# Kernel optimization log

Hardware: AMD Instinct MI355X
Metric: run time of the kernel (lower is better)

Reference implementation:

```python
import jax, jax.numpy as jnp
import numpy as np

DIM = 64
SQRT_DIM = np.sqrt(DIM).astype(np.float32)
NEG_INF = -1e9


def setup_inputs() -> dict:
    key = jax.random.key(0)
    kq, kk, kv, km = jax.random.split(key, 4)
    B, Q, K, D = 32, 1024, 1024, DIM
    query = jax.random.normal(kq, (B, Q, D), dtype=jnp.float32)
    k = jax.random.normal(kk, (B, K, D), dtype=jnp.float32)
    value = jax.random.normal(kv, (B, K, D), dtype=jnp.float32)
    mask = jax.random.randint(km, (B, Q, K), 0, 2).astype(jnp.bool_)
    return {"query": query, "key": k, "value": value, "mask": mask}


def reference(query, key, value, mask):
    # score: [B, Q, K]
    score = jnp.einsum('bqd,bkd->bqk', query, key) / SQRT_DIM
    score = jnp.where(mask, NEG_INF, score)
    attn = jax.nn.softmax(score, axis=-1)
    context = jnp.einsum('bqk,bkd->bqd', attn, value)
    return (context, attn)
```

## Files before the change

kernel.cpp:

```cpp
#include <hip/hip_runtime.h>

constexpr int BATCH = 32;
constexpr int QLEN  = 1024;
constexpr int KLEN  = 1024;
constexpr int DIM   = 64;
constexpr int TQ    = 16;

typedef float    f32x4 __attribute__((ext_vector_type(4)));
typedef int      i32x4 __attribute__((ext_vector_type(4)));
typedef _Float16 f16x8 __attribute__((ext_vector_type(8)));
typedef _Float16 f16x4 __attribute__((ext_vector_type(4)));

__device__ __forceinline__ f16x8 cvt_h8(f32x4 a, f32x4 b) {
  f16x8 h;
  h[0] = (_Float16)a[0]; h[1] = (_Float16)a[1]; h[2] = (_Float16)a[2]; h[3] = (_Float16)a[3];
  h[4] = (_Float16)b[0]; h[5] = (_Float16)b[1]; h[6] = (_Float16)b[2]; h[7] = (_Float16)b[3];
  return h;
}

__device__ __forceinline__ int swz(int r, int c) {
  return (r << 10) + (c ^ ((r & 7) << 3));
}

constexpr int TK = 128;
__global__ __launch_bounds__(256)
void vt_kernel(const float* __restrict__ V, _Float16* __restrict__ Vt) {
  __shared__ _Float16 lt[DIM][TK + 8];
  const int b = blockIdx.y, k0 = blockIdx.x * TK;
  const int t = threadIdx.x;
  const int d4 = (t & 15) * 4;
  #pragma unroll
  for (int p = 0; p < TK / 16; ++p) {
    const int kl = (t >> 4) + p * 16;
    const f32x4 v = *(const f32x4*)(V + ((size_t)(b * KLEN + k0 + kl)) * DIM + d4);
    #pragma unroll
    for (int j = 0; j < 4; ++j) lt[d4 + j][kl] = (_Float16)v[j];
  }
  __syncthreads();
  const int d = t >> 2;
  #pragma unroll
  for (int j2 = 0; j2 < TK / 32; ++j2) {
    const int seg = (t & 3) + j2 * 4;
    *(f16x8*)(Vt + (size_t)b * DIM * KLEN + (size_t)d * KLEN + k0 + seg * 8) =
        *(const f16x8*)(&lt[d][seg * 8]);
  }
}

__global__ __launch_bounds__(256)
void maskpack_kernel(const int* __restrict__ Mg, unsigned long long* __restrict__ Mp) {
  const int l  = threadIdx.x & 63;
  const int gw = blockIdx.x * 4 + (threadIdx.x >> 6);
  for (int row = gw; row < BATCH * QLEN; row += 8192) {
    const int* mr = Mg + (size_t)row * KLEN;
    unsigned long long myw = 0;
    #pragma unroll
    for (int c = 0; c < 4; ++c) {
      const i32x4 v = __builtin_nontemporal_load((const i32x4*)(mr + c * 256 + l * 4));
      #pragma unroll
      for (int u = 0; u < 4; ++u) {
        const unsigned long long bl = __ballot(v[u] != 0);
        if (l == c * 4 + u) myw = bl;
      }
    }
    if (l < 16) Mp[(size_t)row * 16 + l] = myw;
  }
}

__global__ __launch_bounds__(256, 4)
void sdpa_kernel(const float* __restrict__ Qg, const float* __restrict__ Kg,
                 const _Float16* __restrict__ Vt,
                 const unsigned long long* __restrict__ Mp,
                 float* __restrict__ Ctx, float* __restrict__ Attn)
{
  __shared__ __attribute__((aligned(16))) _Float16 sc[TQ * 1024];

  const int tid  = threadIdx.x;
  const int w    = tid >> 6;
  const int l    = tid & 63;
  const int n16  = l & 15;
  const int quad = l >> 4;

  const int lin  = blockIdx.y * gridDim.x + blockIdx.x;
  const int nlin = (lin & 7) * (BATCH * (QLEN / TQ) / 8) + (lin >> 3);
  const int b    = nlin >> 6;
  const int q0   = (nlin & 63) * TQ;

  const float* qbase = Qg + ((size_t)(b * QLEN + q0 + n16)) * DIM + quad * 8;
  const f16x8 aq0 = cvt_h8(*(const f32x4*)(qbase),      *(const f32x4*)(qbase + 4));
  const f16x8 aq1 = cvt_h8(*(const f32x4*)(qbase + 32), *(const f32x4*)(qbase + 36));

  #pragma unroll 4
  for (int kc = 0; kc < 16; ++kc) {
    const int col = w * 256 + kc * 16 + n16;
    const float* kbase = Kg + ((size_t)(b * KLEN + col)) * DIM + quad * 8;
    const f16x8 bk0 = cvt_h8(*(const f32x4*)(kbase),      *(const f32x4*)(kbase + 4));
    const f16x8 bk1 = cvt_h8(*(const f32x4*)(kbase + 32), *(const f32x4*)(kbase + 36));
    f32x4 acc = {0.f, 0.f, 0.f, 0.f};
    acc = __builtin_amdgcn_mfma_f32_16x16x32_f16(aq0, bk0, acc, 0, 0, 0);
    acc = __builtin_amdgcn_mfma_f32_16x16x32_f16(aq1, bk1, acc, 0, 0, 0);
    #pragma unroll
    for (int i = 0; i < 4; ++i)
      sc[swz(quad * 4 + i, col)] = (_Float16)acc[i];
  }
  __syncthreads();

  #pragma unroll
  for (int j = 0; j < 4; ++j) {
    const int r = w * 4 + j;
    const unsigned long long* mpr = Mp + (size_t)(b * QLEN + q0 + r) * 16;
    float s[16];
    float sum = 0.f;
    #pragma unroll
    for (int c = 0; c < 4; ++c) {
      const f16x4 hv = *(const f16x4*)(&sc[swz(r, c * 256 + l * 4)]);
      #pragma unroll
      for (int u = 0; u < 4; ++u) {
        const float e = __expf((float)hv[u] * 0.125f);
        s[c * 4 + u] = ((mpr[c * 4 + u] >> l) & 1ULL) ? 0.f : e;
        sum += s[c * 4 + u];
      }
    }
    #pragma unroll
    for (int d = 1; d < 64; d <<= 1) sum += __shfl_xor(sum, d, 64);
    const float inv = __builtin_amdgcn_rcpf(sum);
    float* arow = Attn + ((size_t)(b * QLEN + q0 + r)) * KLEN;
    #pragma unroll
    for (int c = 0; c < 4; ++c) {
      f32x4 pv = { s[c*4+0] * inv, s[c*4+1] * inv, s[c*4+2] * inv, s[c*4+3] * inv };
      *(f32x4*)(arow + c * 256 + l * 4) = pv;
      f16x4 hp = { (_Float16)pv[0], (_Float16)pv[1], (_Float16)pv[2], (_Float16)pv[3] };
      *(f16x4*)(&sc[swz(r, c * 256 + l * 4)]) = hp;
    }
  }
  __syncthreads();

  const _Float16* vtb = Vt + (size_t)b * DIM * KLEN + (size_t)(w * 16 + n16) * KLEN;
  f32x4 cacc = {0.f, 0.f, 0.f, 0.f};
  #pragma unroll 4
  for (int kk = 0; kk < 32; ++kk) {
    const f16x8 ap = *(const f16x8*)(&sc[swz(n16, kk * 32 + quad * 8)]);
    const f16x8 bv = *(const f16x8*)(vtb + kk * 32 + quad * 8);
    cacc = __builtin_amdgcn_mfma_f32_16x16x32_f16(ap, bv, cacc, 0, 0, 0);
  }
  float* cbase = Ctx + ((size_t)(b * QLEN + q0 + quad * 4)) * DIM + w * 16 + n16;
  #pragma unroll
  for (int i = 0; i < 4; ++i) cbase[(size_t)i * DIM] = cacc[i];
}

extern "C" void kernel_launch(void* const* d_in, const int* in_sizes, int n_in,
                              void* d_out, int out_size, void* d_ws, size_t ws_size,
                              hipStream_t stream) {
  const float* Qg = (const float*)d_in[0];
  const float* Kg = (const float*)d_in[1];
  const float* Vg = (const float*)d_in[2];
  const int*   Mg = (const int*)d_in[3];
  float* Ctx  = (float*)d_out;
  float* Attn = (float*)d_out + (size_t)BATCH * QLEN * DIM;
  _Float16* Vt = (_Float16*)d_ws;
  unsigned long long* Mp =
      (unsigned long long*)((char*)d_ws + (size_t)BATCH * DIM * KLEN * 2);

  dim3 tgrid(KLEN / TK, BATCH);
  vt_kernel<<<tgrid, 256, 0, stream>>>(Vg, Vt);

  maskpack_kernel<<<2048, 256, 0, stream>>>(Mg, Mp);

  dim3 grid(QLEN / TQ, BATCH);
  sdpa_kernel<<<grid, 256, 0, stream>>>(Qg, Kg, Vt, Mp, Ctx, Attn);
}
```

Baseline: 329.3 us.

## Restructure SDPA into single-wave register-resident two-pass softmax with fp16 K

Replaces the 256-thread block that staged a 16x1024 fp16 score tile in LDS with one 64-lane wavefront per 16 query rows. That wavefront computes scores transposed (K as the A operand) and makes two passes: first for the row sums, then it recomputes the scores to write the normalised attention. Probabilities are moved into MFMA A-operand layout with cross-lane shuffles instead of through shared memory. K is pre-converted to fp16 in the V-transpose kernel, and the 1/sqrt(d) scale is folded into Q. The aim is to drop LDS traffic and block-level barriers. The cost is doubled QK^T MFMA work, an extra preprocessing write and read of K, and lower per-block parallelism.

```diff
diff --git a/kernel.cpp b/kernel.cpp
--- a/kernel.cpp
+++ b/kernel.cpp
@@ -10,6 +10,9 @@
 typedef int      i32x4 __attribute__((ext_vector_type(4)));
 typedef _Float16 f16x8 __attribute__((ext_vector_type(8)));
 typedef _Float16 f16x4 __attribute__((ext_vector_type(4)));
+typedef unsigned long long u64;
+typedef unsigned int u32;
+typedef u64 u64x2 __attribute__((ext_vector_type(2)));
 
 __device__ __forceinline__ f16x8 cvt_h8(f32x4 a, f32x4 b) {
   f16x8 h;
@@ -18,13 +21,10 @@
   return h;
 }
 
-__device__ __forceinline__ int swz(int r, int c) {
-  return (r << 10) + (c ^ ((r & 7) << 3));
-}
-
 constexpr int TK = 128;
 __global__ __launch_bounds__(256)
-void vt_kernel(const float* __restrict__ V, _Float16* __restrict__ Vt) {
+void vtkh_kernel(const float* __restrict__ V, const float* __restrict__ Kg,
+                 _Float16* __restrict__ Vt, _Float16* __restrict__ Kh) {
   __shared__ _Float16 lt[DIM][TK + 8];
   const int b = blockIdx.y, k0 = blockIdx.x * TK;
   const int t = threadIdx.x;
@@ -36,6 +36,14 @@
     #pragma unroll
     for (int j = 0; j < 4; ++j) lt[d4 + j][kl] = (_Float16)v[j];
   }
+  #pragma unroll
+  for (int p = 0; p < 8; ++p) {
+    const int idx = t + p * 256;
+    const int kl = idx >> 4, dd = (idx & 15) * 4;
+    const f32x4 v = *(const f32x4*)(Kg + ((size_t)(b * KLEN + k0 + kl)) * DIM + dd);
+    f16x4 h = { (_Float16)v[0], (_Float16)v[1], (_Float16)v[2], (_Float16)v[3] };
+    *(f16x4*)(Kh + ((size_t)(b * KLEN + k0 + kl)) * DIM + dd) = h;
+  }
   __syncthreads();
   const int d = t >> 2;
   #pragma unroll
@@ -47,18 +55,18 @@
 }
 
 __global__ __launch_bounds__(256)
-void maskpack_kernel(const int* __restrict__ Mg, unsigned long long* __restrict__ Mp) {
+void maskpack_kernel(const int* __restrict__ Mg, u64* __restrict__ Mp) {
   const int l  = threadIdx.x & 63;
   const int gw = blockIdx.x * 4 + (threadIdx.x >> 6);
   for (int row = gw; row < BATCH * QLEN; row += 8192) {
     const int* mr = Mg + (size_t)row * KLEN;
-    unsigned long long myw = 0;
+    u64 myw = 0;
     #pragma unroll
     for (int c = 0; c < 4; ++c) {
       const i32x4 v = __builtin_nontemporal_load((const i32x4*)(mr + c * 256 + l * 4));
       #pragma unroll
       for (int u = 0; u < 4; ++u) {
-        const unsigned long long bl = __ballot(v[u] != 0);
+        const u64 bl = __ballot(v[u] != 0);
         if (l == c * 4 + u) myw = bl;
       }
     }
@@ -66,85 +74,111 @@
   }
 }
 
-__global__ __launch_bounds__(256, 4)
-void sdpa_kernel(const float* __restrict__ Qg, const float* __restrict__ Kg,
-                 const _Float16* __restrict__ Vt,
-                 const unsigned long long* __restrict__ Mp,
+__global__ __launch_bounds__(64)
+void sdpa_kernel(const float* __restrict__ Qg, const _Float16* __restrict__ Kh,
+                 const _Float16* __restrict__ Vt, const u64* __restrict__ Mp,
                  float* __restrict__ Ctx, float* __restrict__ Attn)
 {
-  __shared__ __attribute__((aligned(16))) _Float16 sc[TQ * 1024];
-
-  const int tid  = threadIdx.x;
-  const int w    = tid >> 6;
-  const int l    = tid & 63;
+  const int l    = threadIdx.x;
   const int n16  = l & 15;
   const int quad = l >> 4;
 
-  const int lin  = blockIdx.y * gridDim.x + blockIdx.x;
+  const int lin  = blockIdx.x;
   const int nlin = (lin & 7) * (BATCH * (QLEN / TQ) / 8) + (lin >> 3);
   const int b    = nlin >> 6;
   const int q0   = (nlin & 63) * TQ;
 
-  const float* qbase = Qg + ((size_t)(b * QLEN + q0 + n16)) * DIM + quad * 8;
-  const f16x8 aq0 = cvt_h8(*(const f32x4*)(qbase),      *(const f32x4*)(qbase + 4));
-  const f16x8 aq1 = cvt_h8(*(const f32x4*)(qbase + 32), *(const f32x4*)(qbase + 36));
-
-  #pragma unroll 4
-  for (int kc = 0; kc < 16; ++kc) {
-    const int col = w * 256 + kc * 16 + n16;
-    const float* kbase = Kg + ((size_t)(b * KLEN + col)) * DIM + quad * 8;
-    const f16x8 bk0 = cvt_h8(*(const f32x4*)(kbase),      *(const f32x4*)(kbase + 4));
-    const f16x8 bk1 = cvt_h8(*(const f32x4*)(kbase + 32), *(const f32x4*)(kbase + 36));
-    f32x4 acc = {0.f, 0.f, 0.f, 0.f};
-    acc = __builtin_amdgcn_mfma_f32_16x16x32_f16(aq0, bk0, acc, 0, 0, 0);
-    acc = __builtin_amdgcn_mfma_f32_16x16x32_f16(aq1, bk1, acc, 0, 0, 0);
-    #pragma unroll
-    for (int i = 0; i < 4; ++i)
-      sc[swz(quad * 4 + i, col)] = (_Float16)acc[i];
-  }
-  __syncthreads();
-
-  #pragma unroll
-  for (int j = 0; j < 4; ++j) {
-    const int r = w * 4 + j;
-    const unsigned long long* mpr = Mp + (size_t)(b * QLEN + q0 + r) * 16;
-    float s[16];
-    float sum = 0.f;
-    #pragma unroll
-    for (int c = 0; c < 4; ++c) {
-      const f16x4 hv = *(const f16x4*)(&sc[swz(r, c * 256 + l * 4)]);
-      #pragma unroll
-      for (int u = 0; u < 4; ++u) {
-        const float e = __expf((float)hv[u] * 0.125f);
-        s[c * 4 + u] = ((mpr[c * 4 + u] >> l) & 1ULL) ? 0.f : e;
-        sum += s[c * 4 + u];
+  const float* qb = Qg + ((size_t)(b * QLEN + q0 + n16)) * DIM + quad * 8;
+  f32x4 qa0 = *(const f32x4*)(qb),      qa1 = *(const f32x4*)(qb + 4);
+  f32x4 qa2 = *(const f32x4*)(qb + 32), qa3 = *(const f32x4*)(qb + 36);
+  #pragma unroll
+  for (int i = 0; i < 4; ++i) { qa0[i] *= 0.125f; qa1[i] *= 0.125f; qa2[i] *= 0.125f; qa3[i] *= 0.125f; }
+  const f16x8 aq0 = cvt_h8(qa0, qa1);
+  const f16x8 aq1 = cvt_h8(qa2, qa3);
+
+  const _Float16* kb_base = Kh + (size_t)b * KLEN * DIM + quad * 8;
+  const u64* mrow = Mp + ((size_t)(b * QLEN + q0 + n16)) * 16;
+
+  float rsum = 0.f;
+  #pragma unroll
+  for (int g = 0; g < 4; ++g) {
+    const u64x2 w01 = *(const u64x2*)(mrow + g * 4);
+    const u64x2 w23 = *(const u64x2*)(mrow + g * 4 + 2);
+    const u64 w[4] = { w01[0], w01[1], w23[0], w23[1] };
+    #pragma unroll
+    for (int tt = 0; tt < 16; ++tt) {
+      const int t = g * 16 + tt;
+      const _Float16* kp = kb_base + (size_t)(t * 16 + n16) * DIM;
+      const f16x8 ak0 = *(const f16x8*)(kp);
+      const f16x8 ak1 = *(const f16x8*)(kp + 32);
+      f32x4 acc = {0.f, 0.f, 0.f, 0.f};
+      acc = __builtin_amdgcn_mfma_f32_16x16x32_f16(ak0, aq0, acc, 0, 0, 0);
+      acc = __builtin_amdgcn_mfma_f32_16x16x32_f16(ak1, aq1, acc, 0, 0, 0);
+      const u32 sh = tt * 4 + quad;
+      #pragma unroll
+      for (int i = 0; i < 4; ++i)
+        rsum += ((w[i] >> sh) & 1ULL) ? 0.f : __expf(acc[i]);
+    }
+  }
+  rsum += __shfl_xor(rsum, 16, 64);
+  rsum += __shfl_xor(rsum, 32, 64);
+  const float inv = __builtin_amdgcn_rcpf(rsum);
+
+  float* arow = Attn + ((size_t)(b * QLEN + q0 + n16)) * KLEN;
+  const _Float16* vtb = Vt + (size_t)b * DIM * KLEN;
+  f32x4 cacc[4] = { {0.f,0.f,0.f,0.f}, {0.f,0.f,0.f,0.f}, {0.f,0.f,0.f,0.f}, {0.f,0.f,0.f,0.f} };
+  #pragma unroll
+  for (int g = 0; g < 4; ++g) {
+    const u64x2 w01 = *(const u64x2*)(mrow + g * 4);
+    const u64x2 w23 = *(const u64x2*)(mrow + g * 4 + 2);
+    const u64 w[4] = { w01[0], w01[1], w23[0], w23[1] };
+    #pragma unroll
+    for (int m = 0; m < 8; ++m) {
+      uint2 pw[2];
+      #pragma unroll
+      for (int h = 0; h < 2; ++h) {
+        const int t = g * 16 + m * 2 + h;
+        const _Float16* kp = kb_base + (size_t)(t * 16 + n16) * DIM;
+        const f16x8 ak0 = *(const f16x8*)(kp);
+        const f16x8 ak1 = *(const f16x8*)(kp + 32);
+        f32x4 acc = {0.f, 0.f, 0.f, 0.f};
+        acc = __builtin_amdgcn_mfma_f32_16x16x32_f16(ak0, aq0, acc, 0, 0, 0);
+        acc = __builtin_amdgcn_mfma_f32_16x16x32_f16(ak1, aq1, acc, 0, 0, 0);
+        const u32 sh = (t & 15) * 4 + quad;
+        f32x4 e;
+        #pragma unroll
+        for (int i = 0; i < 4; ++i)
+          e[i] = ((w[i] >> sh) & 1ULL) ? 0.f : __expf(acc[i]) * inv;
+        *(f32x4*)(arow + t * 16 + quad * 4) = e;
+        f16x4 ph = { (_Float16)e[0], (_Float16)e[1], (_Float16)e[2], (_Float16)e[3] };
+        __builtin_memcpy(&pw[h], &ph, 8);
+      }
+      const int s0 = n16 + ((quad & 1) << 5);
+      const u32 x0a = (u32)__shfl((int)pw[0].x, s0, 64);
+      const u32 y0a = (u32)__shfl((int)pw[0].y, s0, 64);
+      const u32 x1a = (u32)__shfl((int)pw[1].x, s0, 64);
+      const u32 y1a = (u32)__shfl((int)pw[1].y, s0, 64);
+      const u32 x0b = (u32)__shfl((int)pw[0].x, s0 + 16, 64);
+      const u32 y0b = (u32)__shfl((int)pw[0].y, s0 + 16, 64);
+      const u32 x1b = (u32)__shfl((int)pw[1].x, s0 + 16, 64);
+      const u32 y1b = (u32)__shfl((int)pw[1].y, s0 + 16, 64);
+      const bool hs = (quad & 2) != 0;
+      const u32 dd[4] = { hs ? x1a : x0a, hs ? y1a : y0a,
+                          hs ? x1b : x0b, hs ? y1b : y0b };
+      f16x8 pa; __builtin_memcpy(&pa, dd, 16);
+      const int K0 = g * 256 + m * 32;
+      #pragma unroll
+      for (int dt = 0; dt < 4; ++dt) {
+        const f16x8 bv = *(const f16x8*)(vtb + (size_t)(dt * 16 + n16) * KLEN + K0 + quad * 8);
+        cacc[dt] = __builtin_amdgcn_mfma_f32_16x16x32_f16(pa, bv, cacc[dt], 0, 0, 0);
       }
     }
-    #pragma unroll
-    for (int d = 1; d < 64; d <<= 1) sum += __shfl_xor(sum, d, 64);
-    const float inv = __builtin_amdgcn_rcpf(sum);
-    float* arow = Attn + ((size_t)(b * QLEN + q0 + r)) * KLEN;
-    #pragma unroll
-    for (int c = 0; c < 4; ++c) {
-      f32x4 pv = { s[c*4+0] * inv, s[c*4+1] * inv, s[c*4+2] * inv, s[c*4+3] * inv };
-      *(f32x4*)(arow + c * 256 + l * 4) = pv;
-      f16x4 hp = { (_Float16)pv[0], (_Float16)pv[1], (_Float16)pv[2], (_Float16)pv[3] };
-      *(f16x4*)(&sc[swz(r, c * 256 + l * 4)]) = hp;
-    }
-  }
-  __syncthreads();
-
-  const _Float16* vtb = Vt + (size_t)b * DIM * KLEN + (size_t)(w * 16 + n16) * KLEN;
-  f32x4 cacc = {0.f, 0.f, 0.f, 0.f};
-  #pragma unroll 4
-  for (int kk = 0; kk < 32; ++kk) {
-    const f16x8 ap = *(const f16x8*)(&sc[swz(n16, kk * 32 + quad * 8)]);
-    const f16x8 bv = *(const f16x8*)(vtb + kk * 32 + quad * 8);
-    cacc = __builtin_amdgcn_mfma_f32_16x16x32_f16(ap, bv, cacc, 0, 0, 0);
-  }
-  float* cbase = Ctx + ((size_t)(b * QLEN + q0 + quad * 4)) * DIM + w * 16 + n16;
-  #pragma unroll
-  for (int i = 0; i < 4; ++i) cbase[(size_t)i * DIM] = cacc[i];
+  }
+  #pragma unroll
+  for (int dt = 0; dt < 4; ++dt)
+    #pragma unroll
+    for (int i = 0; i < 4; ++i)
+      Ctx[((size_t)(b * QLEN + q0 + quad * 4 + i)) * DIM + dt * 16 + n16] = cacc[dt][i];
 }
 
 extern "C" void kernel_launch(void* const* d_in, const int* in_sizes, int n_in,
@@ -157,14 +191,14 @@
   float* Ctx  = (float*)d_out;
   float* Attn = (float*)d_out + (size_t)BATCH * QLEN * DIM;
   _Float16* Vt = (_Float16*)d_ws;
-  unsigned long long* Mp =
-      (unsigned long long*)((char*)d_ws + (size_t)BATCH * DIM * KLEN * 2);
+  u64* Mp = (u64*)((char*)d_ws + (size_t)BATCH * DIM * KLEN * 2);
+  _Float16* Kh = (_Float16*)((char*)d_ws + (size_t)BATCH * DIM * KLEN * 2 +
+                             (size_t)BATCH * QLEN * 16 * 8);
 
   dim3 tgrid(KLEN / TK, BATCH);
-  vt_kernel<<<tgrid, 256, 0, stream>>>(Vg, Vt);
+  vtkh_kernel<<<tgrid, 256, 0, stream>>>(Vg, Kg, Vt, Kh);
 
   maskpack_kernel<<<2048, 256, 0, stream>>>(Mg, Mp);
 
-  dim3 grid(QLEN / TQ, BATCH);
-  sdpa_kernel<<<grid, 256, 0, stream>>>(Qg, Kg, Vt, Mp, Ctx, Attn);
-}
+  sdpa_kernel<<<2048, 64, 0, stream>>>(Qg, Kh, Vt, Mp, Ctx, Attn);
+}
```

Measured after the change: 332.2 us. Within noise of the previous version (+0.9%).
